# Kernel tuning notes

Measured on AMD Instinct MI355X. Metric: run time of the kernel, lower is better.

The kernel has to match this reference:

```python
import jax, jax.numpy as jnp
import numpy as np
import math

B, S, D, H, DH, R = 2, 2048, 1024, 16, 64, 8
EPS = 1e-5


def setup_inputs() -> dict:
    key = jax.random.key(0)
    ks = jax.random.split(key, 8)
    hidden_states = jax.random.normal(ks[0], (B, S, D), jnp.float32)
    # causal boolean mask (batch, seq, seq); every row has >=1 valid entry
    causal = jnp.tril(jnp.ones((S, S), dtype=bool))
    attention_mask = jnp.broadcast_to(causal, (B, S, S))
    # lora: (n_layers=1, 4, batch, hidden, rank); [0]=qA,[1]=kA,[2]=qB,[3]=kB
    lora = jax.random.normal(ks[1], (1, 4, B, D, R), jnp.float32) * 0.02
    ln_w = jnp.ones((D,), jnp.float32)
    Wq = jax.random.normal(ks[2], (D, D), jnp.float32) * 0.02
    Wk = jax.random.normal(ks[3], (D, D), jnp.float32) * 0.02
    Wv = jax.random.normal(ks[4], (D, D), jnp.float32) * 0.02
    Wo = jax.random.normal(ks[5], (D, D), jnp.float32) * 0.02
    return dict(hidden_states=hidden_states, attention_mask=attention_mask,
                lora=lora, ln_w=ln_w, Wq=Wq, Wk=Wk, Wv=Wv, Wo=Wo)


def _rms_ln(x, w):
    # model_center LayerNorm with bias=False == RMS layernorm
    var = jnp.mean(x * x, axis=-1, keepdims=True)
    return x * jax.lax.rsqrt(var + EPS) * w


def _lora_delta(h, A, Bm):
    # h: (b,s,D), A: (b,D,R), Bm: (b,R,D);  h + (h@A)@Bm * 2
    z = jnp.einsum('bsd,bdr->bsr', h, A)
    return h + jnp.einsum('bsr,brd->bsd', z, Bm) * 2


def reference(hidden_states, attention_mask, lora, ln_w, Wq, Wk, Wv, Wo):
    b, s, _ = hidden_states.shape
    x = _rms_ln(hidden_states, ln_w)
    h_q = x @ Wq.T
    h_k = x @ Wk.T
    h_v = x @ Wv.T
    layer = lora[0]  # (4, b, D, R)
    h_q = _lora_delta(h_q, layer[0], jnp.swapaxes(layer[2], 1, 2))
    h_k = _lora_delta(h_k, layer[1], jnp.swapaxes(layer[3], 1, 2))
    q = h_q.reshape(b, s, H, DH)
    k = h_k.reshape(b, s, H, DH)
    v = h_v.reshape(b, s, H, DH)
    score = jnp.einsum('bqhd,bkhd->bhqk', q, k) / math.sqrt(DH)
    m = attention_mask[:, None, :, :]  # (b,1,s,s)
    score = jnp.where(m, score, -jnp.inf)
    p = jax.nn.softmax(score, axis=-1)
    p = jnp.where(m, p, jnp.float32(0))
    out = jnp.einsum('bhqk,bkhd->bqhd', p, v).reshape(b, s, H * DH)
    out = out @ Wo.T
    return hidden_states + out
```

## Files before the change

kernel.cpp:

```cpp
#include <hip/hip_runtime.h>

typedef __bf16 bf16;
typedef __bf16 bf16x4 __attribute__((ext_vector_type(4)));
typedef __bf16 bf16x8 __attribute__((ext_vector_type(8)));
typedef float f32x4 __attribute__((ext_vector_type(4)));

#define DM 1024
#define NROW 4096
#define SEQ 2048
#define HDIM 64
#define NEGBIG -30000.0f

#define SWB(base, row, bcol) \
  ((char*)(base) + (row) * 128 + ((bcol) ^ (((row) & 7) << 4)))

__device__ __forceinline__ void async16(const bf16* g, bf16* l) {
  __builtin_amdgcn_global_load_lds(
      (const __attribute__((address_space(1))) unsigned int*)g,
      (__attribute__((address_space(3))) unsigned int*)l, 16, 0, 0);
}

template <int MODE>
__device__ __forceinline__ void gemm128(bf16* __restrict__ sA,
                                        bf16* __restrict__ sB,
                                        const bf16* __restrict__ A,
                                        const bf16* __restrict__ Bw,
                                        bf16* __restrict__ Cb,
                                        int m0, int n0) {
  const int t = threadIdx.x;
  const int lane = t & 63;
  const int w = t >> 6;
  const int wm = (w & 1) * 64;
  const int wn = (w >> 1) * 64;
  const int lr = lane & 15;
  const int kg = lane >> 4;

  f32x4 acc[4][4];
#pragma unroll
  for (int i = 0; i < 4; i++)
#pragma unroll
    for (int j = 0; j < 4; j++)
#pragma unroll
      for (int r = 0; r < 4; r++) acc[i][j][r] = 0.0f;

  const int srow = t >> 2;
  const int scol = (t & 3) * 8;
  const bf16* gA = A + (size_t)(m0 + srow) * DM + scol;
  const bf16* gB = Bw + (size_t)(n0 + srow) * DM + scol;

#define GSTAGE(k0_, buf_)                                          \
  {                                                                \
    async16(gA + (k0_), &sA[(buf_)*4096 + t * 8]);                 \
    async16(gA + (k0_) + 64 * DM, &sA[(buf_)*4096 + t * 8 + 2048]);\
    async16(gB + (k0_), &sB[(buf_)*4096 + t * 8]);                 \
    async16(gB + (k0_) + 64 * DM, &sB[(buf_)*4096 + t * 8 + 2048]);\
  }

  GSTAGE(0, 0);
  GSTAGE(32, 1);

  int cur = 0;
  for (int k0 = 0; k0 < DM; k0 += 32) {
    const int n2 = (cur == 0) ? 2 : cur - 1;
    if (k0 + 64 < DM) {
      GSTAGE(k0 + 64, n2);
      asm volatile("s_waitcnt vmcnt(8)" ::: "memory");
    } else if (k0 + 32 < DM) {
      asm volatile("s_waitcnt vmcnt(4)" ::: "memory");
    } else {
      asm volatile("s_waitcnt vmcnt(0)" ::: "memory");
    }
    __builtin_amdgcn_s_barrier();

    bf16x8 av[4], bv[4];
#pragma unroll
    for (int mi = 0; mi < 4; mi++)
      av[mi] = *(const bf16x8*)&sA[cur * 4096 + (wm + mi * 16 + lr) * 32 + kg * 8];
#pragma unroll
    for (int nj = 0; nj < 4; nj++)
      bv[nj] = *(const bf16x8*)&sB[cur * 4096 + (wn + nj * 16 + lr) * 32 + kg * 8];
    __builtin_amdgcn_s_setprio(1);
#pragma unroll
    for (int mi = 0; mi < 4; mi++)
#pragma unroll
      for (int nj = 0; nj < 4; nj++)
        acc[mi][nj] = __builtin_amdgcn_mfma_f32_16x16x32_bf16(av[mi], bv[nj],
                                                              acc[mi][nj], 0, 0, 0);
    __builtin_amdgcn_s_setprio(0);
    __builtin_amdgcn_s_barrier();
    cur = (cur == 2) ? 0 : cur + 1;
  }
#undef GSTAGE

  if (MODE == 2) {
    const int bb2 = m0 >> 11;
    const int sbase = (m0 & 2047) + wm + kg * 4;
#pragma unroll
    for (int mi = 0; mi < 4; mi++) {
#pragma unroll
      for (int nj = 0; nj < 4; nj++) {
        bf16x4 o;
#pragma unroll
        for (int r = 0; r < 4; r++) o[r] = (bf16)acc[mi][nj][r];
        const int col = n0 + wn + nj * 16 + lr;
        bf16* dst = Cb + ((size_t)(bb2 * 1024 + col)) * SEQ + sbase + mi * 16;
        *(bf16x4*)dst = o;
      }
    }
    return;
  }

#pragma unroll
  for (int mi = 0; mi < 4; mi++) {
#pragma unroll
    for (int r = 0; r < 4; r++) {
      const int grow = m0 + wm + mi * 16 + kg * 4 + r;
      const size_t base = (size_t)grow * DM + n0 + wn + lr;
#pragma unroll
      for (int nj = 0; nj < 4; nj++)
        Cb[base + nj * 16] = (bf16)acc[mi][nj][r];
    }
  }
}

__global__ __launch_bounds__(256) void k_pre(const float* __restrict__ hin,
                                             const float* __restrict__ wln,
                                             const float* __restrict__ Wq,
                                             const float* __restrict__ Wk,
                                             const float* __restrict__ Wv,
                                             const float* __restrict__ Wo,
                                             bf16* __restrict__ xo,
                                             bf16* __restrict__ wcast) {
  __shared__ float red[4];
  const int t = threadIdx.x;
  const int bb = blockIdx.x;
  if (bb < NROW) {
    const int row = bb;
    const float4 h4 = ((const float4*)(hin + (size_t)row * DM))[t];
    float ss = h4.x * h4.x + h4.y * h4.y + h4.z * h4.z + h4.w * h4.w;
#pragma unroll
    for (int off = 1; off < 64; off <<= 1) ss += __shfl_xor(ss, off, 64);
    if ((t & 63) == 0) red[t >> 6] = ss;
    __syncthreads();
    ss = red[0] + red[1] + red[2] + red[3];
    const float inv = rsqrtf(ss * (1.0f / DM) + 1e-5f);
    const float4 w4 = ((const float4*)wln)[t];
    bf16x4 o;
    o[0] = (bf16)(h4.x * inv * w4.x);
    o[1] = (bf16)(h4.y * inv * w4.y);
    o[2] = (bf16)(h4.z * inv * w4.z);
    o[3] = (bf16)(h4.w * inv * w4.w);
    *(bf16x4*)&xo[(size_t)row * DM + t * 4] = o;
  } else {
    const int i = (bb - NROW) * 256 + t;
    const int mat = i >> 18;
    const int off = i & 262143;
    const float* s = (mat == 0) ? Wq : (mat == 1) ? Wk : (mat == 2) ? Wv : Wo;
    const float4 v = ((const float4*)s)[off];
    bf16x4 o;
    o[0] = (bf16)v.x; o[1] = (bf16)v.y; o[2] = (bf16)v.z; o[3] = (bf16)v.w;
    ((bf16x4*)wcast)[i] = o;
  }
}

__global__ __launch_bounds__(256) void k_qkv(const bf16* __restrict__ x,
                                             const bf16* __restrict__ Wq,
                                             const bf16* __restrict__ Wk,
                                             const bf16* __restrict__ Wv,
                                             bf16* __restrict__ hq,
                                             bf16* __restrict__ hk,
                                             bf16* __restrict__ hvT) {
  __shared__ __align__(16) bf16 sA[3 * 128 * 32];
  __shared__ __align__(16) bf16 sB[3 * 128 * 32];
  const int nb = blockIdx.y;
  const int wsel = nb >> 3;
  const int n0 = (nb & 7) * 128;
  const int m0 = blockIdx.x * 128;
  if (wsel == 2) {
    gemm128<2>(sA, sB, x, Wv, hvT, m0, n0);
  } else {
    gemm128<0>(sA, sB, x, (wsel == 0) ? Wq : Wk, (wsel == 0) ? hq : hk, m0, n0);
  }
}

__global__ __launch_bounds__(256) void k_oproj(const bf16* __restrict__ ctx,
                                               const bf16* __restrict__ Wo,
                                               const float* __restrict__ resid,
                                               float* __restrict__ out) {
  __shared__ __align__(16) bf16 sA[3 * 128 * 32];
  __shared__ __align__(16) bf16 sB[3 * 64 * 32];
  const int t = threadIdx.x;
  const int lane = t & 63;
  const int w = t >> 6;
  const int wm = (w & 1) * 64;
  const int wn = (w >> 1) * 32;
  const int lr = lane & 15;
  const int kg = lane >> 4;
  const int m0 = blockIdx.x * 128;
  const int n0 = blockIdx.y * 64;

  f32x4 acc[4][2];
#pragma unroll
  for (int i = 0; i < 4; i++)
#pragma unroll
    for (int j = 0; j < 2; j++)
#pragma unroll
      for (int r = 0; r < 4; r++) acc[i][j][r] = 0.0f;

  const int srow = t >> 2;
  const int scol = (t & 3) * 8;
  const bf16* gA = ctx + (size_t)(m0 + srow) * DM + scol;
  const bf16* gB = Wo + (size_t)(n0 + srow) * DM + scol;

#define GSTAGE3(k0_, buf_)                                         \
  {                                                                \
    async16(gA + (k0_), &sA[(buf_)*4096 + t * 8]);                 \
    async16(gA + (k0_) + 64 * DM, &sA[(buf_)*4096 + t * 8 + 2048]);\
    async16(gB + (k0_), &sB[(buf_)*2048 + t * 8]);                 \
  }

  GSTAGE3(0, 0);
  GSTAGE3(32, 1);

  int cur = 0;
  for (int k0 = 0; k0 < DM; k0 += 32) {
    const int n2 = (cur == 0) ? 2 : cur - 1;
    if (k0 + 64 < DM) {
      GSTAGE3(k0 + 64, n2);
      asm volatile("s_waitcnt vmcnt(6)" ::: "memory");
    } else if (k0 + 32 < DM) {
      asm volatile("s_waitcnt vmcnt(3)" ::: "memory");
    } else {
      asm volatile("s_waitcnt vmcnt(0)" ::: "memory");
    }
    __builtin_amdgcn_s_barrier();

    bf16x8 av[4], bv[2];
#pragma unroll
    for (int mi = 0; mi < 4; mi++)
      av[mi] = *(const bf16x8*)&sA[cur * 4096 + (wm + mi * 16 + lr) * 32 + kg * 8];
#pragma unroll
    for (int nj = 0; nj < 2; nj++)
      bv[nj] = *(const bf16x8*)&sB[cur * 2048 + (wn + nj * 16 + lr) * 32 + kg * 8];
    __builtin_amdgcn_s_setprio(1);
#pragma unroll
    for (int mi = 0; mi < 4; mi++)
#pragma unroll
      for (int nj = 0; nj < 2; nj++)
        acc[mi][nj] = __builtin_amdgcn_mfma_f32_16x16x32_bf16(av[mi], bv[nj],
                                                              acc[mi][nj], 0, 0, 0);
    __builtin_amdgcn_s_setprio(0);
    __builtin_amdgcn_s_barrier();
    cur = (cur == 2) ? 0 : cur + 1;
  }
#undef GSTAGE3

#pragma unroll
  for (int mi = 0; mi < 4; mi++) {
#pragma unroll
    for (int r = 0; r < 4; r++) {
      const int grow = m0 + wm + mi * 16 + kg * 4 + r;
      const size_t base = (size_t)grow * DM + n0 + wn + lr;
#pragma unroll
      for (int nj = 0; nj < 2; nj++)
        out[base + nj * 16] = acc[mi][nj][r] + resid[base + nj * 16];
    }
  }
}

__global__ __launch_bounds__(256) void k_mid(bf16* __restrict__ hq,
                                             bf16* __restrict__ hk,
                                             const float* __restrict__ lora) {
  __shared__ __align__(16) char smem[18432];
  const int t = threadIdx.x;
  const int lid = blockIdx.x;
  const int lane = t & 63;
  const int w = t >> 6;
  const int lr = lane & 15;
  const int kg = lane >> 4;

  bf16* At = (bf16*)smem;
  float* Zp = (float*)(smem + 16384);
  const int row0 = (lid & 127) * 32;
  const int which = lid >> 7;
  const int b = row0 >> 11;
  bf16* H = (which == 0 ? hq : hk) + (size_t)row0 * DM;
  const float* Am = lora + (size_t)(which == 0 ? 0 : 1) * 16384 + (size_t)b * 8192;
  const float* Bm = lora + (size_t)(which == 0 ? 2 : 3) * 16384 + (size_t)b * 8192;

  const int d0 = lane * 16;
  float4 Bv[32];
  {
    const float4* bp = (const float4*)(Bm + (size_t)d0 * 8);
#pragma unroll
    for (int i = 0; i < 32; i++) Bv[i] = bp[i];
  }

  {
    const float4* ap = (const float4*)(Am + (size_t)t * 32);
#pragma unroll
    for (int i = 0; i < 8; i++) {
      const float4 v = ap[i];
      const int idx = t * 32 + i * 4;
      At[(idx & 7) * 1024 + (idx >> 3)]             = (bf16)v.x;
      At[((idx + 1) & 7) * 1024 + ((idx + 1) >> 3)] = (bf16)v.y;
      At[((idx + 2) & 7) * 1024 + ((idx + 2) >> 3)] = (bf16)v.z;
      At[((idx + 3) & 7) * 1024 + ((idx + 3) >> 3)] = (bf16)v.w;
    }
  }
  __syncthreads();

  const int tile = w & 1;
  const int khalf = w >> 1;
  {
    f32x4 zacc;
#pragma unroll
    for (int r = 0; r < 4; r++) zacc[r] = 0.f;
    const bf16* gH = H + (size_t)(tile * 16 + lr) * DM + khalf * 512 + kg * 8;
    const bf16* lA = &At[(lr & 7) * 1024 + khalf * 512 + kg * 8];
#pragma unroll
    for (int i = 0; i < 16; i++) {
      const bf16x8 ah = *(const bf16x8*)(gH + i * 32);
      const bf16x8 ba = *(const bf16x8*)(lA + i * 32);
      zacc = __builtin_amdgcn_mfma_f32_16x16x32_bf16(ah, ba, zacc, 0, 0, 0);
    }
    if (lr < 8) {
#pragma unroll
      for (int r = 0; r < 4; r++)
        Zp[(khalf * 32 + tile * 16 + kg * 4 + r) * 8 + lr] = zacc[r];
    }
  }
  __syncthreads();

#pragma unroll
  for (int rr = 0; rr < 8; rr++) {
    const int row = w * 8 + rr;
    const float4 z0 = *(const float4*)&Zp[(row) * 8 + 0];
    const float4 z1 = *(const float4*)&Zp[(row) * 8 + 4];
    const float4 y0 = *(const float4*)&Zp[(32 + row) * 8 + 0];
    const float4 y1 = *(const float4*)&Zp[(32 + row) * 8 + 4];
    const float za = z0.x + y0.x, zb = z0.y + y0.y, zc = z0.z + y0.z, zd = z0.w + y0.w;
    const float ze = z1.x + y1.x, zf = z1.y + y1.y, zg = z1.z + y1.z, zh = z1.w + y1.w;
    bf16* hp = H + (size_t)row * DM + d0;
    const bf16x8 h0 = *(const bf16x8*)hp;
    const bf16x8 h1 = *(const bf16x8*)(hp + 8);
    bf16x8 o0, o1;
#pragma unroll
    for (int j = 0; j < 16; j++) {
      const float4 b0 = Bv[2 * j];
      const float4 b1 = Bv[2 * j + 1];
      const float delta = za * b0.x + zb * b0.y + zc * b0.z + zd * b0.w +
                          ze * b1.x + zf * b1.y + zg * b1.z + zh * b1.w;
      const float hj = (j < 8) ? (float)h0[j] : (float)h1[j - 8];
      const bf16 ov = (bf16)(hj + 2.0f * delta);
      if (j < 8) o0[j] = ov; else o1[j - 8] = ov;
    }
    *(bf16x8*)hp = o0;
    *(bf16x8*)(hp + 8) = o1;
  }
}

__global__ __launch_bounds__(256, 4) void k_attn(const bf16* __restrict__ hq,
                                                 const bf16* __restrict__ hk,
                                                 const bf16* __restrict__ hvT,
                                                 bf16* __restrict__ ctx) {
  const int n = blockIdx.x;
  const int slab = n & 31;
  const int hh = slab & 15;
  const int b = slab >> 4;
  const int xx = n >> 5;
  const int s = xx >> 3;
  const int v = xx & 7;
  const int qt = (s == 0) ? 4 * v : (s == 1) ? 31 - 4 * v
               : (s == 2) ? 4 * v + 2 : 29 - 4 * v;
  const int qbase = qt * 64;

  const int t = threadIdx.x;
  const int lane = t & 63;
  const int w = t >> 6;
  const int lr = lane & 15;
  const int kg = lane >> 4;

  __shared__ __align__(16) bf16 sK[64 * 64];
  __shared__ __align__(16) bf16 sVt[64 * 64];
  __shared__ __align__(16) bf16 sP[64 * 64];

  const size_t rowbase = (size_t)b * SEQ;
  const int hoff = hh * HDIM;
  const float sscale = 0.18033688011112042f;

  bf16x8 bq0, bq1;
  {
    const bf16* gQ = hq + (rowbase + qbase + w * 16 + lr) * DM + hoff + kg * 8;
    const bf16x8 q0 = *(const bf16x8*)gQ;
    const bf16x8 q1 = *(const bf16x8*)(gQ + 32);
#pragma unroll
    for (int j = 0; j < 8; j++) {
      bq0[j] = (bf16)((float)q0[j] * sscale);
      bq1[j] = (bf16)((float)q1[j] * sscale);
    }
  }

  const int r4 = t >> 2;
  const int ce = (t & 3) * 16;
  const int cb = (t & 3) * 32;
  const bf16* gK = hk + (rowbase + r4) * DM + hoff + ce;
  const bf16* gV = hvT + ((size_t)slab * HDIM + r4) * SEQ + ce;
  bf16x8 kr0 = *(const bf16x8*)gK;
  bf16x8 kr1 = *(const bf16x8*)(gK + 8);
  bf16x8 vr0 = *(const bf16x8*)gV;
  bf16x8 vr1 = *(const bf16x8*)(gV + 8);

  float m_l = NEGBIG, l_l = 0.f;
  f32x4 oacc[4];
#pragma unroll
  for (int nj = 0; nj < 4; nj++)
#pragma unroll
    for (int r = 0; r < 4; r++) oacc[nj][r] = 0.f;

  for (int kt = 0; kt <= qt; kt++) {
    *(bf16x8*)SWB(sK, r4, cb) = kr0;
    *(bf16x8*)SWB(sK, r4, cb + 16) = kr1;
    *(bf16x8*)SWB(sVt, r4, cb) = vr0;
    *(bf16x8*)SWB(sVt, r4, cb + 16) = vr1;
    __syncthreads();

    if (kt < qt) {
      const bf16* gK2 = gK + (size_t)(kt + 1) * 64 * DM;
      const bf16* gV2 = gV + (kt + 1) * 64;
      kr0 = *(const bf16x8*)gK2;
      kr1 = *(const bf16x8*)(gK2 + 8);
      vr0 = *(const bf16x8*)gV2;
      vr1 = *(const bf16x8*)(gV2 + 8);
    }

    f32x4 sc[4];
#pragma unroll
    for (int nj = 0; nj < 4; nj++)
#pragma unroll
      for (int r = 0; r < 4; r++) sc[nj][r] = 0.f;
    __builtin_amdgcn_s_setprio(1);
#pragma unroll
    for (int ks = 0; ks < 2; ks++) {
      const bf16x8 bq = ks ? bq1 : bq0;
#pragma unroll
      for (int nj = 0; nj < 4; nj++) {
        const bf16x8 ak = *(const bf16x8*)SWB(sK, nj * 16 + lr, ks * 64 + kg * 16);
        sc[nj] = __builtin_amdgcn_mfma_f32_16x16x32_bf16(ak, bq, sc[nj], 0, 0, 0);
      }
    }
    __builtin_amdgcn_s_setprio(0);

    if (kt == qt) {
      const int ql = w * 16 + lr;
#pragma unroll
      for (int nj = 0; nj < 4; nj++)
#pragma unroll
        for (int r = 0; r < 4; r++) {
          const int kl = nj * 16 + kg * 4 + r;
          sc[nj][r] = (kl <= ql) ? sc[nj][r] : NEGBIG;
        }
    }

    float rm = sc[0][0];
#pragma unroll
    for (int nj = 0; nj < 4; nj++)
#pragma unroll
      for (int r = 0; r < 4; r++) rm = fmaxf(rm, sc[nj][r]);
    rm = fmaxf(rm, __shfl_xor(rm, 16, 64));
    rm = fmaxf(rm, __shfl_xor(rm, 32, 64));

    const bool skip = __all(rm - m_l <= 8.0f);
    if (!skip) {
      const float mnew = fmaxf(m_l, rm);
      const float alpha = __builtin_amdgcn_exp2f(m_l - mnew);
      l_l *= alpha;
      m_l = mnew;
#pragma unroll
      for (int r = 0; r < 4; r++) {
        const float ar = __shfl(alpha, (lane & 48) | (kg * 4 + r), 64);
#pragma unroll
        for (int nj = 0; nj < 4; nj++) oacc[nj][r] *= ar;
      }
    }

    float rs = 0.f;
#pragma unroll
    for (int nj = 0; nj < 4; nj++)
#pragma unroll
      for (int r = 0; r < 4; r++) {
        const float p = __builtin_amdgcn_exp2f(sc[nj][r] - m_l);
        sc[nj][r] = p;
        rs += p;
      }
    rs += __shfl_xor(rs, 16, 64);
    rs += __shfl_xor(rs, 32, 64);
    l_l += rs;

#pragma unroll
    for (int nj = 0; nj < 4; nj++) {
      bf16x4 p4;
#pragma unroll
      for (int r = 0; r < 4; r++) p4[r] = (bf16)sc[nj][r];
      *(bf16x4*)SWB(sP, w * 16 + lr, nj * 32 + kg * 8) = p4;
    }

    __builtin_amdgcn_s_setprio(1);
#pragma unroll
    for (int ks = 0; ks < 2; ks++) {
      const bf16x8 ap = *(const bf16x8*)SWB(sP, w * 16 + lr, ks * 64 + kg * 16);
#pragma unroll
      for (int nj = 0; nj < 4; nj++) {
        const bf16x8 bv = *(const bf16x8*)SWB(sVt, nj * 16 + lr, ks * 64 + kg * 16);
        oacc[nj] = __builtin_amdgcn_mfma_f32_16x16x32_bf16(ap, bv, oacc[nj], 0, 0, 0);
      }
    }
    __builtin_amdgcn_s_setprio(0);
    __syncthreads();
  }

#pragma unroll
  for (int r = 0; r < 4; r++) {
    const float lrow = __shfl(l_l, (lane & 48) | (kg * 4 + r), 64);
    const float invl = 1.0f / lrow;
    const int qr = qbase + w * 16 + kg * 4 + r;
    const size_t base = (rowbase + qr) * DM + hoff + lr;
#pragma unroll
    for (int nj = 0; nj < 4; nj++)
      ctx[base + nj * 16] = (bf16)(oacc[nj][r] * invl);
  }
}

extern "C" void kernel_launch(void* const* d_in, const int* in_sizes, int n_in,
                              void* d_out, int out_size, void* d_ws, size_t ws_size,
                              hipStream_t stream) {
  const float* hidden = (const float*)d_in[0];
  const float* lora = (const float*)d_in[2];
  const float* wln  = (const float*)d_in[3];
  const float* Wq   = (const float*)d_in[4];
  const float* Wk   = (const float*)d_in[5];
  const float* Wv   = (const float*)d_in[6];
  const float* Wo   = (const float*)d_in[7];
  float* out = (float*)d_out;

  const size_t BUF = (size_t)NROW * DM;
  if (ws_size < 4 * BUF * sizeof(bf16)) return;
  bf16* ws = (bf16*)d_ws;
  bf16* hq  = ws;
  bf16* hk  = ws + 1 * BUF;
  bf16* hvT = ws + 2 * BUF;
  bf16* ctx = ws + 3 * BUF;

  bf16* dob = (bf16*)d_out;
  bf16* x   = dob;
  bf16* wqb = dob + BUF;
  bf16* wkb = dob + BUF + DM * DM;
  bf16* wvb = dob + BUF + 2 * DM * DM;
  bf16* wob = dob + BUF + 3 * DM * DM;

  k_pre<<<dim3(2 * NROW), dim3(256), 0, stream>>>(hidden, wln, Wq, Wk, Wv, Wo, x, wqb);
  k_qkv<<<dim3(32, 24), dim3(256), 0, stream>>>(x, wqb, wkb, wvb, hq, hk, hvT);
  k_mid<<<dim3(256), dim3(256), 0, stream>>>(hq, hk, lora);
  k_attn<<<dim3(1024), dim3(256), 0, stream>>>(hq, hk, hvT, ctx);
  k_oproj<<<dim3(32, 16), dim3(256), 0, stream>>>(ctx, wob, hidden, out);
}
```

Before: 211.1 us.

## Split long causal attention tiles across two blocks and merge partials

Query tiles at or above a threshold are split along the key dimension into two blocks, each writing fp32 partial outputs and running max/sum stats into scratch space reused from the output buffer. A new merge kernel combines the two halves with rescaling and writes the bf16 context. A lookup table orders blocks longest first to balance the causal workload, and the occupancy hint rises from 4 to 6. In exchange it adds an extra launch and fp32 partial traffic, and it depends on the reused scratch regions (x and the q/k weight copies) being dead by the time attention runs.

```diff
diff --git a/kernel.cpp b/kernel.cpp
--- a/kernel.cpp
+++ b/kernel.cpp
@@ -10,9 +10,21 @@
 #define SEQ 2048
 #define HDIM 64
 #define NEGBIG -30000.0f
+#define SPLIT_QT 20
 
 #define SWB(base, row, bcol) \
   ((char*)(base) + (row) * 128 + ((bcol) ^ (((row) & 7) << 4)))
+
+__constant__ unsigned char ATT_LUT[44] = {
+    38, 36, 34, 32,
+    62, 63, 60, 30,
+    61, 58, 59, 56, 28,
+    57, 54, 55, 52, 26,
+    53, 50, 51, 48, 24,
+    49, 46, 47, 44, 22,
+    45, 42, 43, 40, 20,
+    41, 18,
+    16, 14, 12, 10, 8, 6, 4, 2, 0};
 
 __device__ __forceinline__ void async16(const bf16* g, bf16* l) {
   __builtin_amdgcn_global_load_lds(
@@ -360,19 +372,23 @@
   }
 }
 
-__global__ __launch_bounds__(256, 4) void k_attn(const bf16* __restrict__ hq,
+__global__ __launch_bounds__(256, 6) void k_attn(const bf16* __restrict__ hq,
                                                  const bf16* __restrict__ hk,
                                                  const bf16* __restrict__ hvT,
-                                                 bf16* __restrict__ ctx) {
+                                                 bf16* __restrict__ ctx,
+                                                 float* __restrict__ pbuf,
+                                                 float* __restrict__ mlbuf) {
   const int n = blockIdx.x;
   const int slab = n & 31;
   const int hh = slab & 15;
   const int b = slab >> 4;
-  const int xx = n >> 5;
-  const int s = xx >> 3;
-  const int v = xx & 7;
-  const int qt = (s == 0) ? 4 * v : (s == 1) ? 31 - 4 * v
-               : (s == 2) ? 4 * v + 2 : 29 - 4 * v;
+  const int code = ATT_LUT[n >> 5];
+  const int qt = code >> 1;
+  const int seg = code & 1;
+  const bool split = (qt >= SPLIT_QT);
+  const int h = (qt + 2) >> 1;
+  const int k0t = split ? seg * h : 0;
+  const int k1t = (split && seg == 0) ? h : qt + 1;
   const int qbase = qt * 64;
 
   const int t = threadIdx.x;
@@ -406,10 +422,10 @@
   const int cb = (t & 3) * 32;
   const bf16* gK = hk + (rowbase + r4) * DM + hoff + ce;
   const bf16* gV = hvT + ((size_t)slab * HDIM + r4) * SEQ + ce;
-  bf16x8 kr0 = *(const bf16x8*)gK;
-  bf16x8 kr1 = *(const bf16x8*)(gK + 8);
-  bf16x8 vr0 = *(const bf16x8*)gV;
-  bf16x8 vr1 = *(const bf16x8*)(gV + 8);
+  bf16x8 kr0 = *(const bf16x8*)(gK + (size_t)k0t * 64 * DM);
+  bf16x8 kr1 = *(const bf16x8*)(gK + (size_t)k0t * 64 * DM + 8);
+  bf16x8 vr0 = *(const bf16x8*)(gV + k0t * 64);
+  bf16x8 vr1 = *(const bf16x8*)(gV + k0t * 64 + 8);
 
   float m_l = NEGBIG, l_l = 0.f;
   f32x4 oacc[4];
@@ -418,14 +434,14 @@
 #pragma unroll
     for (int r = 0; r < 4; r++) oacc[nj][r] = 0.f;
 
-  for (int kt = 0; kt <= qt; kt++) {
+  for (int kt = k0t; kt < k1t; kt++) {
     *(bf16x8*)SWB(sK, r4, cb) = kr0;
     *(bf16x8*)SWB(sK, r4, cb + 16) = kr1;
     *(bf16x8*)SWB(sVt, r4, cb) = vr0;
     *(bf16x8*)SWB(sVt, r4, cb + 16) = vr1;
     __syncthreads();
 
-    if (kt < qt) {
+    if (kt + 1 < k1t) {
       const bf16* gK2 = gK + (size_t)(kt + 1) * 64 * DM;
       const bf16* gV2 = gV + (kt + 1) * 64;
       kr0 = *(const bf16x8*)gK2;
@@ -519,15 +535,68 @@
     __syncthreads();
   }
 
-#pragma unroll
-  for (int r = 0; r < 4; r++) {
-    const float lrow = __shfl(l_l, (lane & 48) | (kg * 4 + r), 64);
-    const float invl = 1.0f / lrow;
-    const int qr = qbase + w * 16 + kg * 4 + r;
-    const size_t base = (rowbase + qr) * DM + hoff + lr;
-#pragma unroll
-    for (int nj = 0; nj < 4; nj++)
-      ctx[base + nj * 16] = (bf16)(oacc[nj][r] * invl);
+  if (split) {
+    const int pid = (qt - SPLIT_QT) * 32 + slab;
+    float* PO = pbuf + (size_t)pid * 8192 + seg * 4096;
+#pragma unroll
+    for (int r = 0; r < 4; r++) {
+      const int qloc = w * 16 + kg * 4 + r;
+#pragma unroll
+      for (int nj = 0; nj < 4; nj++)
+        PO[qloc * 64 + nj * 16 + lr] = oacc[nj][r];
+    }
+    if (kg == 0) {
+      float* ml = mlbuf + (size_t)pid * 256 + seg * 128 + (w * 16 + lr) * 2;
+      ml[0] = m_l;
+      ml[1] = l_l;
+    }
+  } else {
+#pragma unroll
+    for (int r = 0; r < 4; r++) {
+      const float lrow = __shfl(l_l, (lane & 48) | (kg * 4 + r), 64);
+      const float invl = 1.0f / lrow;
+      const int qr = qbase + w * 16 + kg * 4 + r;
+      const size_t base = (rowbase + qr) * DM + hoff + lr;
+#pragma unroll
+      for (int nj = 0; nj < 4; nj++)
+        ctx[base + nj * 16] = (bf16)(oacc[nj][r] * invl);
+    }
+  }
+}
+
+__global__ __launch_bounds__(256) void k_amerge(const float* __restrict__ pbuf,
+                                                const float* __restrict__ mlbuf,
+                                                bf16* __restrict__ ctx) {
+  const int pid = blockIdx.x;
+  const int qt = SPLIT_QT + (pid >> 5);
+  const int slab = pid & 31;
+  const int hh = slab & 15;
+  const int b = slab >> 4;
+  const int t = threadIdx.x;
+  const int row = t >> 2;
+  const int c0 = (t & 3) * 16;
+
+  const float* ml0 = mlbuf + (size_t)pid * 256 + row * 2;
+  const float m0 = ml0[0], l0 = ml0[1];
+  const float m1 = ml0[128], l1 = ml0[129];
+  const float m = fmaxf(m0, m1);
+  const float a0 = __builtin_amdgcn_exp2f(m0 - m);
+  const float a1 = __builtin_amdgcn_exp2f(m1 - m);
+  const float invl = 1.0f / (a0 * l0 + a1 * l1);
+
+  const float* p0 = pbuf + (size_t)pid * 8192 + row * 64 + c0;
+  const float* p1 = p0 + 4096;
+  bf16* dst = ctx + ((size_t)b * SEQ + qt * 64 + row) * DM + hh * HDIM + c0;
+#pragma unroll
+  for (int i = 0; i < 4; i++) {
+    const float4 v0 = *(const float4*)(p0 + i * 4);
+    const float4 v1 = *(const float4*)(p1 + i * 4);
+    bf16x4 o;
+    o[0] = (bf16)((a0 * v0.x + a1 * v1.x) * invl);
+    o[1] = (bf16)((a0 * v0.y + a1 * v1.y) * invl);
+    o[2] = (bf16)((a0 * v0.z + a1 * v1.z) * invl);
+    o[3] = (bf16)((a0 * v0.w + a1 * v1.w) * invl);
+    *(bf16x4*)(dst + i * 4) = o;
   }
 }
 
@@ -557,10 +626,13 @@
   bf16* wkb = dob + BUF + DM * DM;
   bf16* wvb = dob + BUF + 2 * DM * DM;
   bf16* wob = dob + BUF + 3 * DM * DM;
+  float* pbuf  = (float*)dob;
+  float* mlbuf = (float*)(dob + BUF + 2 * DM * DM);
 
   k_pre<<<dim3(2 * NROW), dim3(256), 0, stream>>>(hidden, wln, Wq, Wk, Wv, Wo, x, wqb);
   k_qkv<<<dim3(32, 24), dim3(256), 0, stream>>>(x, wqb, wkb, wvb, hq, hk, hvT);
   k_mid<<<dim3(256), dim3(256), 0, stream>>>(hq, hk, lora);
-  k_attn<<<dim3(1024), dim3(256), 0, stream>>>(hq, hk, hvT, ctx);
+  k_attn<<<dim3(1408), dim3(256), 0, stream>>>(hq, hk, hvT, ctx, pbuf, mlbuf);
+  k_amerge<<<dim3(384), dim3(256), 0, stream>>>(pbuf, mlbuf, ctx);
   k_oproj<<<dim3(32, 16), dim3(256), 0, stream>>>(ctx, wob, hidden, out);
 }
```

Measured after the change: 244.1 us. 1.16x slower.
